# Performance work log

Hardware: AMD Instinct MI355X
Metric: run time of the kernel (lower is better)

Reference implementation:

```python
import jax, jax.numpy as jnp
import numpy as np

H = 4  # heads
L = 2  # num_layers


def _segment_softmax(alpha, seg, num_segments):
    # alpha: [E, H], seg: [E] destination node ids
    m = jax.ops.segment_max(alpha, seg, num_segments=num_segments)  # [N, H]
    m = jnp.where(jnp.isfinite(m), m, 0.0)
    ex = jnp.exp(alpha - m[seg])
    s = jax.ops.segment_sum(ex, seg, num_segments=num_segments)  # [N, H]
    return ex / (s[seg] + 1e-16)


def _conv(x, src, dst, edge_weight, edge_attr, wq, wk, wv, we, g, b):
    # x: [N, D]; edge_attr: [E, D]; one WePredConv layer (eval mode, no dropout)
    N, D = x.shape
    C = D // H
    q = (x @ wq).reshape(N, H, C)
    k = (x @ wk).reshape(N, H, C)
    v = (x @ wv).reshape(N, H, C)
    e = (edge_attr @ we).reshape(-1, H, C)
    alpha = (q[dst] + k[src] + e).sum(-1) / jnp.sqrt(jnp.float32(C))  # [E, H]
    alpha = alpha + g[None, :] * edge_weight[:, None]
    alpha = jax.nn.leaky_relu(alpha, negative_slope=0.2)
    alpha = _segment_softmax(alpha, dst, N)
    msg = v[src] * alpha[:, :, None]  # [E, H, C]
    out = jax.ops.segment_sum(msg, dst, num_segments=N).reshape(N, H * C)
    return out + b


def setup_inputs() -> dict:
    key = jax.random.key(0)
    ks = jax.random.split(key, 12)
    N, E, D, F, R = 50000, 400000, 128, 256, 200
    sc = 0.08  # ~xavier scale
    return {
        "entity": jnp.arange(N, dtype=jnp.int32),
        "edge_index": jax.random.randint(ks[0], (2, E), 0, N, dtype=jnp.int32),
        "edge_type": jax.random.randint(ks[1], (E,), 0, R, dtype=jnp.int32),
        "edge_weight": jax.random.uniform(ks[2], (E,), dtype=jnp.float32),
        "ent_table": jax.random.normal(ks[3], (N, F), dtype=jnp.float32),
        "proj_w": jax.random.normal(ks[4], (F, D), dtype=jnp.float32) * sc,
        "proj_b": jnp.zeros((D,), dtype=jnp.float32),
        "rel_emb": jax.random.normal(ks[5], (R, D), dtype=jnp.float32) * sc,
        "Wq": jax.random.normal(ks[6], (L, D, D), dtype=jnp.float32) * sc,
        "Wk": jax.random.normal(ks[7], (L, D, D), dtype=jnp.float32) * sc,
        "Wv": jax.random.normal(ks[8], (L, D, D), dtype=jnp.float32) * sc,
        "We": jax.random.normal(ks[9], (L, D, D), dtype=jnp.float32) * sc,
        "gate": jnp.ones((L, H), dtype=jnp.float32),
        "conv_bias": jnp.zeros((L, D), dtype=jnp.float32),
    }


def reference(entity, edge_index, edge_type, edge_weight, ent_table, proj_w,
              proj_b, rel_emb, Wq, Wk, Wv, We, gate, conv_bias):
    src, dst = edge_index[0], edge_index[1]
    x = ent_table[entity] @ proj_w + proj_b          # [N, D]
    edge_attr = rel_emb[edge_type]                   # [E, D]
    for l in range(L):
        x = _conv(x, src, dst, edge_weight, edge_attr,
                  Wq[l], Wk[l], Wv[l], We[l], gate[l], conv_bias[l])
        if l != L - 1:
            x = jax.nn.elu(x)
    return x
```

## Files before the change

### kernel.cpp

```cpp
#include <hip/hip_runtime.h>
#include <hip/hip_fp16.h>

#define HD 4
#define DD 128
#define CC 32
#define SCAN_B 64
#define SCAN_T 256

typedef float  f32x4   __attribute__((ext_vector_type(4)));
typedef short  short8v __attribute__((ext_vector_type(8)));

__device__ __forceinline__ unsigned short f2bf(float x) {
    unsigned u = __float_as_uint(x);
    return (unsigned short)((u + 0x7FFFu + ((u >> 16) & 1u)) >> 16);
}
__device__ __forceinline__ float bf2f(unsigned short h) {
    return __uint_as_float((unsigned)h << 16);
}

__global__ __launch_bounds__(256) void prep_kernel(
    const float* __restrict__ Wq, const float* __restrict__ Wk,
    const float* __restrict__ We, const float* __restrict__ rel,
    float* __restrict__ Wqh, float* __restrict__ Wkh,
    float* __restrict__ esum, int R)
{
    __shared__ float WehS[2][DD][HD];
    int tid = threadIdx.x;
    for (int i = tid; i < 2 * DD * HD; i += 256) {
        int l = i / (DD * HD);
        int d = (i / HD) % DD;
        int h = i % HD;
        const float* bq = Wq + ((size_t)l * DD + d) * DD + h * CC;
        const float* bk = Wk + ((size_t)l * DD + d) * DD + h * CC;
        const float* be = We + ((size_t)l * DD + d) * DD + h * CC;
        float sq = 0.f, sk = 0.f, se = 0.f;
        for (int c = 0; c < CC; ++c) { sq += bq[c]; sk += bk[c]; se += be[c]; }
        if (blockIdx.x == 0) { Wqh[i] = sq; Wkh[i] = sk; }
        WehS[l][d][h] = se;
    }
    __syncthreads();
    for (int i = blockIdx.x * 256 + tid; i < 2 * R * HD; i += gridDim.x * 256) {
        int l = i / (R * HD);
        int r = (i / HD) % R;
        int h = i % HD;
        const float* rp = rel + (size_t)r * DD;
        float a = 0.f;
        for (int d = 0; d < DD; ++d) a += rp[d] * WehS[l][d][h];
        esum[i] = a;
    }
}

__global__ __launch_bounds__(256) void prep_bt(
    const float* __restrict__ pw, const float* __restrict__ Wv,
    unsigned short* __restrict__ btp, unsigned short* __restrict__ btv)
{
    int t = blockIdx.x * 256 + threadIdx.x;
    if (t < 128 * 256) {
        int col = t >> 8, k = t & 255;
        btp[(size_t)col * 256 + k] = f2bf(pw[(size_t)k * DD + col]);
    } else if (t < 128 * 256 + 2 * DD * DD) {
        int u = t - 128 * 256;
        int l = u >> 14;
        int r = u & 16383;
        int col = r >> 7, k = r & 127;
        btv[((size_t)l * DD + col) * DD + k] = f2bf(Wv[((size_t)l * DD + k) * DD + col]);
    }
}

__global__ __launch_bounds__(256) void gemm_mfma(
    const float* __restrict__ A, const int* __restrict__ gather,
    const unsigned short* __restrict__ bth, const float* __restrict__ bias,
    const float* __restrict__ Wqh, const float* __restrict__ Wkh,
    float* __restrict__ Cf, __half* __restrict__ Chf,
    float* __restrict__ qs, float* __restrict__ ks,
    int M, int K)
{
    __shared__ unsigned short AhL[4][4][64][8];
    __shared__ unsigned short AlL[4][4][64][8];
    __shared__ unsigned short BhL[4][8][64][8];
    __shared__ float wq[DD * HD], wk[DD * HD];

    const int tid = threadIdx.x;
    const int wave = tid >> 6, lane = tid & 63;
    const int row0 = blockIdx.x * 64;

    if (qs) {
        for (int i = tid; i < DD * HD; i += 256) { wq[i] = Wqh[i]; wk[i] = Wkh[i]; }
    }

    const int sr = tid >> 2;
    const int sks = tid & 3;
    int arow = row0 + sr; if (arow >= M) arow = M - 1;
    const int ga = gather ? gather[arow] : arow;
    const float* Ap = A + (size_t)ga * K + sks * 32;

    const int bc = tid >> 1;
    const int bh2 = (tid & 1) * 64;
    const unsigned short* Bp = bth + (size_t)bc * K + bh2;
    const int bct = bc >> 4, bfr = bc & 15;

    const int fr = lane & 15, fg = lane >> 4;

    f32x4 acc[8] = {};
    float qp[4] = {}, kp[4] = {};

    const int nch = K >> 7;
    for (int ch = 0; ch < nch; ++ch) {
        float4 a[8];
#pragma unroll
        for (int i = 0; i < 8; ++i) a[i] = *(const float4*)(Ap + ch * 128 + i * 4);
        short8v b[8];
#pragma unroll
        for (int i = 0; i < 8; ++i) b[i] = *(const short8v*)(Bp + ch * 128 + i * 8);

        if (ch) __syncthreads();

        {
            const int rt = sr >> 4, frr = sr & 15;
#pragma unroll
            for (int g = 0; g < 4; ++g) {
                float vv[8] = {a[g*2].x, a[g*2].y, a[g*2].z, a[g*2].w,
                               a[g*2+1].x, a[g*2+1].y, a[g*2+1].z, a[g*2+1].w};
                short8v hv, lv;
#pragma unroll
                for (int j = 0; j < 8; ++j) {
                    unsigned short h = f2bf(vv[j]);
                    hv[j] = (short)h;
                    lv[j] = (short)f2bf(vv[j] - bf2f(h));
                }
                *(short8v*)&AhL[rt][sks][g * 16 + frr][0] = hv;
                *(short8v*)&AlL[rt][sks][g * 16 + frr][0] = lv;
            }
        }
        if (qs) {
#pragma unroll
            for (int i = 0; i < 8; ++i) {
                const float arr[4] = {a[i].x, a[i].y, a[i].z, a[i].w};
#pragma unroll
                for (int j = 0; j < 4; ++j) {
                    int d = ch * 128 + sks * 32 + i * 4 + j;
                    float4 qw = *(const float4*)&wq[d * HD];
                    float4 kw = *(const float4*)&wk[d * HD];
                    qp[0] += arr[j] * qw.x; qp[1] += arr[j] * qw.y;
                    qp[2] += arr[j] * qw.z; qp[3] += arr[j] * qw.w;
                    kp[0] += arr[j] * kw.x; kp[1] += arr[j] * kw.y;
                    kp[2] += arr[j] * kw.z; kp[3] += arr[j] * kw.w;
                }
            }
        }
#pragma unroll
        for (int g = 0; g < 8; ++g) {
            int kk = bh2 + g * 8;
            int ksb = kk >> 5, fgb = (kk & 31) >> 3;
            *(short8v*)&BhL[ksb][bct][fgb * 16 + bfr][0] = b[g];
        }
        __syncthreads();

#pragma unroll
        for (int ksc = 0; ksc < 4; ++ksc) {
            short8v ah = *(const short8v*)&AhL[wave][ksc][lane][0];
            short8v al = *(const short8v*)&AlL[wave][ksc][lane][0];
#pragma unroll
            for (int c = 0; c < 8; ++c) {
                short8v bh = *(const short8v*)&BhL[ksc][c][lane][0];
                acc[c] = __builtin_amdgcn_mfma_f32_16x16x32_bf16(ah, bh, acc[c], 0, 0, 0);
                acc[c] = __builtin_amdgcn_mfma_f32_16x16x32_bf16(al, bh, acc[c], 0, 0, 0);
            }
        }
    }

    if (qs) {
#pragma unroll
        for (int off = 1; off < 4; off <<= 1) {
#pragma unroll
            for (int h = 0; h < 4; ++h) {
                qp[h] += __shfl_xor(qp[h], off, 64);
                kp[h] += __shfl_xor(kp[h], off, 64);
            }
        }
        if ((tid & 3) == 0) {
            int row = row0 + sr;
            if (row < M) {
                *(float4*)&qs[(size_t)row * HD] = make_float4(qp[0], qp[1], qp[2], qp[3]);
                *(float4*)&ks[(size_t)row * HD] = make_float4(kp[0], kp[1], kp[2], kp[3]);
            }
        }
    }

#pragma unroll
    for (int c = 0; c < 8; ++c) {
        float bv = bias ? bias[c * 16 + fr] : 0.f;
#pragma unroll
        for (int i = 0; i < 4; ++i) {
            int row = row0 + wave * 16 + fg * 4 + i;
            if (row < M) {
                float val = acc[c][i] + bv;
                if (Chf) Chf[(size_t)row * DD + c * 16 + fr] = __float2half(val);
                else     Cf [(size_t)row * DD + c * 16 + fr] = val;
            }
        }
    }
}

__global__ __launch_bounds__(256) void csr_count(
    const int* __restrict__ dstv, int* __restrict__ deg, int E)
{
    int t = blockIdx.x * 256 + threadIdx.x;
    if (t < E) atomicAdd(&deg[dstv[t]], 1);
}

__global__ __launch_bounds__(SCAN_T) void scan_partial(
    const int* __restrict__ deg, int* __restrict__ blksum, int N)
{
    __shared__ int red[SCAN_T];
    int chunk = (N + SCAN_B - 1) / SCAN_B;
    int b0 = blockIdx.x * chunk;
    int e0 = b0 + chunk; if (e0 > N) e0 = N;
    int s = 0;
    for (int i = b0 + threadIdx.x; i < e0; i += SCAN_T) s += deg[i];
    red[threadIdx.x] = s;
    __syncthreads();
    for (int off = SCAN_T / 2; off > 0; off >>= 1) {
        if (threadIdx.x < off) red[threadIdx.x] += red[threadIdx.x + off];
        __syncthreads();
    }
    if (threadIdx.x == 0) blksum[blockIdx.x] = red[0];
}

__global__ __launch_bounds__(64) void scan_blk(
    const int* __restrict__ blksum, int* __restrict__ blkoff)
{
    if (threadIdx.x == 0) {
        int acc = 0;
        for (int i = 0; i < SCAN_B; ++i) { blkoff[i] = acc; acc += blksum[i]; }
        blkoff[SCAN_B] = acc;
    }
}

__global__ __launch_bounds__(SCAN_T) void scan_final(
    const int* __restrict__ deg, const int* __restrict__ blkoff,
    int* __restrict__ row_ptr, int N)
{
    __shared__ int tsum[SCAN_T];
    int tid = threadIdx.x;
    int chunk = (N + SCAN_B - 1) / SCAN_B;
    int b0 = blockIdx.x * chunk;
    int e0 = b0 + chunk; if (e0 > N) e0 = N;
    int tchunk = (chunk + SCAN_T - 1) / SCAN_T;
    int tb = b0 + tid * tchunk;
    int te = tb + tchunk; if (te > e0) te = e0;
    int s = 0;
    for (int i = tb; i < te; ++i) s += deg[i];
    tsum[tid] = s;
    __syncthreads();
    for (int off = 1; off < SCAN_T; off <<= 1) {
        int v = (tid >= off) ? tsum[tid - off] : 0;
        __syncthreads();
        tsum[tid] += v;
        __syncthreads();
    }
    int base = blkoff[blockIdx.x] + ((tid == 0) ? 0 : tsum[tid - 1]);
    for (int i = tb; i < te; ++i) { row_ptr[i] = base; base += deg[i]; }
    if (blockIdx.x == SCAN_B - 1 && tid == SCAN_T - 1) row_ptr[N] = blkoff[SCAN_B];
}

__global__ __launch_bounds__(256) void csr_scatter(
    const int* __restrict__ srcv, const int* __restrict__ dstv,
    const int* __restrict__ etype, const float* __restrict__ ew,
    const int* __restrict__ row_ptr, int* __restrict__ cursor,
    int4* __restrict__ c_pack, int E)
{
    int e = blockIdx.x * 256 + threadIdx.x;
    if (e >= E) return;
    int d = dstv[e];
    int p = row_ptr[d] + atomicAdd(&cursor[d], 1);
    c_pack[p] = make_int4(srcv[e], etype[e], __float_as_int(ew[e]), 0);
}

__global__ __launch_bounds__(256) void fused_conv(
    const int* __restrict__ row_ptr, const int4* __restrict__ c_pack,
    const float* __restrict__ qs, const float* __restrict__ ks,
    const float* __restrict__ esum, const float* __restrict__ gate,
    const __half* __restrict__ v, const float* __restrict__ bias,
    float* __restrict__ out, int N, int do_elu)
{
    int gw = (blockIdx.x * 256 + threadIdx.x) >> 6;
    int lane = threadIdx.x & 63;
    if (gw >= N) return;
    const int n = gw;
    const int beg = row_ptr[n], end = row_ptr[n + 1];
    const int c0 = lane * 2;
    const int h = lane >> 4;
    const float L2E = 1.4426950408889634f;
    const float scL = 0.17677669529663687f * 1.4426950408889634f;
    const float qh = qs[(size_t)n * HD + h];
    const float ghL = gate[h] * L2E;

    float num0 = 0.f, num1 = 0.f, den = 0.f;

    int j = beg;
    for (; j + 8 <= end; j += 8) {
        int4 p[8];
#pragma unroll
        for (int u = 0; u < 8; ++u) p[u] = c_pack[j + u];
        float kh[8], eh[8];
        float2 vv[8];
#pragma unroll
        for (int u = 0; u < 8; ++u) kh[u] = ks[(size_t)p[u].x * HD + h];
#pragma unroll
        for (int u = 0; u < 8; ++u) eh[u] = esum[(size_t)p[u].y * HD + h];
#pragma unroll
        for (int u = 0; u < 8; ++u)
            vv[u] = __half22float2(*(const __half2*)&v[(size_t)p[u].x * DD + c0]);
#pragma unroll
        for (int u = 0; u < 8; ++u) {
            float a = (qh + kh[u] + eh[u]) * scL + ghL * __int_as_float(p[u].z);
            a = a > 0.f ? a : 0.2f * a;
            float e = exp2f(a);
            den += e;
            num0 = fmaf(e, vv[u].x, num0);
            num1 = fmaf(e, vv[u].y, num1);
        }
    }
    for (; j + 4 <= end; j += 4) {
        int4 p0 = c_pack[j];
        int4 p1 = c_pack[j + 1];
        int4 p2 = c_pack[j + 2];
        int4 p3 = c_pack[j + 3];
        float kh0 = ks[(size_t)p0.x * HD + h];
        float kh1 = ks[(size_t)p1.x * HD + h];
        float kh2 = ks[(size_t)p2.x * HD + h];
        float kh3 = ks[(size_t)p3.x * HD + h];
        float eh0 = esum[(size_t)p0.y * HD + h];
        float eh1 = esum[(size_t)p1.y * HD + h];
        float eh2 = esum[(size_t)p2.y * HD + h];
        float eh3 = esum[(size_t)p3.y * HD + h];
        float2 vv0 = __half22float2(*(const __half2*)&v[(size_t)p0.x * DD + c0]);
        float2 vv1 = __half22float2(*(const __half2*)&v[(size_t)p1.x * DD + c0]);
        float2 vv2 = __half22float2(*(const __half2*)&v[(size_t)p2.x * DD + c0]);
        float2 vv3 = __half22float2(*(const __half2*)&v[(size_t)p3.x * DD + c0]);
        float a0 = (qh + kh0 + eh0) * scL + ghL * __int_as_float(p0.z);
        float a1 = (qh + kh1 + eh1) * scL + ghL * __int_as_float(p1.z);
        float a2 = (qh + kh2 + eh2) * scL + ghL * __int_as_float(p2.z);
        float a3 = (qh + kh3 + eh3) * scL + ghL * __int_as_float(p3.z);
        a0 = a0 > 0.f ? a0 : 0.2f * a0;
        a1 = a1 > 0.f ? a1 : 0.2f * a1;
        a2 = a2 > 0.f ? a2 : 0.2f * a2;
        a3 = a3 > 0.f ? a3 : 0.2f * a3;
        float e0 = exp2f(a0), e1 = exp2f(a1);
        float e2 = exp2f(a2), e3 = exp2f(a3);
        den += (e0 + e1) + (e2 + e3);
        num0 = fmaf(e0, vv0.x, num0); num1 = fmaf(e0, vv0.y, num1);
        num0 = fmaf(e1, vv1.x, num0); num1 = fmaf(e1, vv1.y, num1);
        num0 = fmaf(e2, vv2.x, num0); num1 = fmaf(e2, vv2.y, num1);
        num0 = fmaf(e3, vv3.x, num0); num1 = fmaf(e3, vv3.y, num1);
    }
    for (; j < end; ++j) {
        int4 cur = c_pack[j];
        float kh = ks[(size_t)cur.x * HD + h];
        float eh = esum[(size_t)cur.y * HD + h];
        float2 vv = __half22float2(*(const __half2*)&v[(size_t)cur.x * DD + c0]);
        float a = (qh + kh + eh) * scL + ghL * __int_as_float(cur.z);
        a = a > 0.f ? a : 0.2f * a;
        float e = exp2f(a);
        den += e;
        num0 = fmaf(e, vv.x, num0);
        num1 = fmaf(e, vv.y, num1);
    }

    float inv = 1.f / (den + 1e-16f);
    float r0 = num0 * inv + bias[c0];
    float r1 = num1 * inv + bias[c0 + 1];
    if (do_elu) {
        r0 = r0 > 0.f ? r0 : expm1f(r0);
        r1 = r1 > 0.f ? r1 : expm1f(r1);
    }
    *(float2*)&out[(size_t)n * DD + c0] = make_float2(r0, r1);
}

extern "C" void kernel_launch(void* const* d_in, const int* in_sizes, int n_in,
                              void* d_out, int out_size, void* d_ws, size_t ws_size,
                              hipStream_t stream)
{
    const int*   entity = (const int*)d_in[0];
    const int*   eidx   = (const int*)d_in[1];
    const int*   etype  = (const int*)d_in[2];
    const float* ew     = (const float*)d_in[3];
    const float* ent    = (const float*)d_in[4];
    const float* pw     = (const float*)d_in[5];
    const float* pb     = (const float*)d_in[6];
    const float* rel    = (const float*)d_in[7];
    const float* Wq     = (const float*)d_in[8];
    const float* Wk     = (const float*)d_in[9];
    const float* Wv     = (const float*)d_in[10];
    const float* We     = (const float*)d_in[11];
    const float* gate   = (const float*)d_in[12];
    const float* cb     = (const float*)d_in[13];

    const int N = in_sizes[0];
    const int E = in_sizes[2];
    const int F = in_sizes[4] / N;
    const int R = in_sizes[7] / DD;

    const int* srcv = eidx;
    const int* dstv = eidx + E;

    float* ws = (float*)d_ws;
    size_t o = 0;
    float* xbuf    = ws + o; o += (size_t)N * DD;
    __half* vbuf   = (__half*)(ws + o); o += (size_t)N * DD / 2;
    float* qs      = ws + o; o += (size_t)N * HD;
    float* ks      = ws + o; o += (size_t)N * HD;
    float* Wqh     = ws + o; o += 2 * DD * HD;
    float* Wkh     = ws + o; o += 2 * DD * HD;
    float* esum    = ws + o; o += (size_t)2 * R * HD;
    int*   deg     = (int*)(ws + o); o += N;
    int*   cursor  = (int*)(ws + o); o += N;
    int*   row_ptr = (int*)(ws + o); o += (size_t)N + 1;
    int*   blksum  = (int*)(ws + o); o += SCAN_B;
    int*   blkoff  = (int*)(ws + o); o += SCAN_B + 1;
    o = (o + 3) & ~(size_t)3;
    int4*  c_pack  = (int4*)(ws + o); o += (size_t)E * 4;
    unsigned short* btp = (unsigned short*)(ws + o); o += 128 * 256 / 2;
    unsigned short* btv = (unsigned short*)(ws + o); o += 2 * DD * DD / 2;

    prep_kernel<<<16, 256, 0, stream>>>(Wq, Wk, We, rel, Wqh, Wkh, esum, R);
    prep_bt<<<(128 * 256 + 2 * DD * DD + 255) / 256, 256, 0, stream>>>(
        pw, Wv, btp, btv);

    hipMemsetAsync(deg, 0, (size_t)2 * N * sizeof(int), stream);
    csr_count<<<(E + 255) / 256, 256, 0, stream>>>(dstv, deg, E);
    scan_partial<<<SCAN_B, SCAN_T, 0, stream>>>(deg, blksum, N);
    scan_blk<<<1, 64, 0, stream>>>(blksum, blkoff);
    scan_final<<<SCAN_B, SCAN_T, 0, stream>>>(deg, blkoff, row_ptr, N);
    csr_scatter<<<(E + 255) / 256, 256, 0, stream>>>(
        srcv, dstv, etype, ew, row_ptr, cursor, c_pack, E);

    const int gblk = (N + 63) / 64;
    gemm_mfma<<<gblk, 256, 0, stream>>>(
        ent, entity, btp, pb, nullptr, nullptr,
        xbuf, nullptr, nullptr, nullptr, N, F);

    const int fblk = (N + 3) / 4;
    for (int l = 0; l < 2; ++l) {
        gemm_mfma<<<gblk, 256, 0, stream>>>(
            xbuf, nullptr, btv + (size_t)l * DD * DD, nullptr,
            Wqh + l * DD * HD, Wkh + l * DD * HD,
            nullptr, vbuf, qs, ks, N, DD);
        fused_conv<<<fblk, 256, 0, stream>>>(
            row_ptr, c_pack, qs, ks, esum + (size_t)l * R * HD,
            gate + l * HD, vbuf, cb + l * DD,
            (l == 0) ? xbuf : (float*)d_out, N, (l == 0) ? 1 : 0);
    }
}
```

Measured before the change: 236.4 us.

## Precompute per-edge attention bias in a separate pass before fused conv

New measurement: 226.8 us. 4.1% less time.

```diff
diff --git a/kernel.cpp b/kernel.cpp
--- a/kernel.cpp
+++ b/kernel.cpp
@@ -268,19 +268,41 @@
     const int* __restrict__ srcv, const int* __restrict__ dstv,
     const int* __restrict__ etype, const float* __restrict__ ew,
     const int* __restrict__ row_ptr, int* __restrict__ cursor,
-    int4* __restrict__ c_pack, int E)
+    int4* __restrict__ c_pack, int* __restrict__ c_src, int E)
 {
     int e = blockIdx.x * 256 + threadIdx.x;
     if (e >= E) return;
     int d = dstv[e];
     int p = row_ptr[d] + atomicAdd(&cursor[d], 1);
     c_pack[p] = make_int4(srcv[e], etype[e], __float_as_int(ew[e]), 0);
+    c_src[p] = srcv[e];
+}
+
+__global__ __launch_bounds__(256) void edge_prep(
+    const int4* __restrict__ c_pack, const float* __restrict__ ks,
+    const float* __restrict__ esum, const float* __restrict__ gate,
+    float4* __restrict__ bedge, int E)
+{
+    int t = blockIdx.x * 256 + threadIdx.x;
+    if (t >= E) return;
+    const float L2E = 1.4426950408889634f;
+    const float scL = 0.17677669529663687f * 1.4426950408889634f;
+    int4 p = c_pack[t];
+    float w = __int_as_float(p.z);
+    float4 kv = *(const float4*)&ks[(size_t)p.x * HD];
+    float4 ev = *(const float4*)&esum[(size_t)p.y * HD];
+    float4 g  = *(const float4*)gate;
+    float4 b;
+    b.x = (kv.x + ev.x) * scL + g.x * L2E * w;
+    b.y = (kv.y + ev.y) * scL + g.y * L2E * w;
+    b.z = (kv.z + ev.z) * scL + g.z * L2E * w;
+    b.w = (kv.w + ev.w) * scL + g.w * L2E * w;
+    bedge[t] = b;
 }
 
 __global__ __launch_bounds__(256) void fused_conv(
-    const int* __restrict__ row_ptr, const int4* __restrict__ c_pack,
-    const float* __restrict__ qs, const float* __restrict__ ks,
-    const float* __restrict__ esum, const float* __restrict__ gate,
+    const int* __restrict__ row_ptr, const int* __restrict__ c_src,
+    const float* __restrict__ bedge, const float* __restrict__ qs,
     const __half* __restrict__ v, const float* __restrict__ bias,
     float* __restrict__ out, int N, int do_elu)
 {
@@ -291,30 +313,24 @@
     const int beg = row_ptr[n], end = row_ptr[n + 1];
     const int c0 = lane * 2;
     const int h = lane >> 4;
-    const float L2E = 1.4426950408889634f;
     const float scL = 0.17677669529663687f * 1.4426950408889634f;
-    const float qh = qs[(size_t)n * HD + h];
-    const float ghL = gate[h] * L2E;
+    const float qhs = qs[(size_t)n * HD + h] * scL;
 
     float num0 = 0.f, num1 = 0.f, den = 0.f;
 
     int j = beg;
     for (; j + 8 <= end; j += 8) {
-        int4 p[8];
-#pragma unroll
-        for (int u = 0; u < 8; ++u) p[u] = c_pack[j + u];
-        float kh[8], eh[8];
-        float2 vv[8];
-#pragma unroll
-        for (int u = 0; u < 8; ++u) kh[u] = ks[(size_t)p[u].x * HD + h];
-#pragma unroll
-        for (int u = 0; u < 8; ++u) eh[u] = esum[(size_t)p[u].y * HD + h];
+        int s[8]; float bh[8]; float2 vv[8];
+#pragma unroll
+        for (int u = 0; u < 8; ++u) s[u] = c_src[j + u];
+#pragma unroll
+        for (int u = 0; u < 8; ++u) bh[u] = bedge[(size_t)(j + u) * HD + h];
 #pragma unroll
         for (int u = 0; u < 8; ++u)
-            vv[u] = __half22float2(*(const __half2*)&v[(size_t)p[u].x * DD + c0]);
+            vv[u] = __half22float2(*(const __half2*)&v[(size_t)s[u] * DD + c0]);
 #pragma unroll
         for (int u = 0; u < 8; ++u) {
-            float a = (qh + kh[u] + eh[u]) * scL + ghL * __int_as_float(p[u].z);
+            float a = qhs + bh[u];
             a = a > 0.f ? a : 0.2f * a;
             float e = exp2f(a);
             den += e;
@@ -323,26 +339,16 @@
         }
     }
     for (; j + 4 <= end; j += 4) {
-        int4 p0 = c_pack[j];
-        int4 p1 = c_pack[j + 1];
-        int4 p2 = c_pack[j + 2];
-        int4 p3 = c_pack[j + 3];
-        float kh0 = ks[(size_t)p0.x * HD + h];
-        float kh1 = ks[(size_t)p1.x * HD + h];
-        float kh2 = ks[(size_t)p2.x * HD + h];
-        float kh3 = ks[(size_t)p3.x * HD + h];
-        float eh0 = esum[(size_t)p0.y * HD + h];
-        float eh1 = esum[(size_t)p1.y * HD + h];
-        float eh2 = esum[(size_t)p2.y * HD + h];
-        float eh3 = esum[(size_t)p3.y * HD + h];
-        float2 vv0 = __half22float2(*(const __half2*)&v[(size_t)p0.x * DD + c0]);
-        float2 vv1 = __half22float2(*(const __half2*)&v[(size_t)p1.x * DD + c0]);
-        float2 vv2 = __half22float2(*(const __half2*)&v[(size_t)p2.x * DD + c0]);
-        float2 vv3 = __half22float2(*(const __half2*)&v[(size_t)p3.x * DD + c0]);
-        float a0 = (qh + kh0 + eh0) * scL + ghL * __int_as_float(p0.z);
-        float a1 = (qh + kh1 + eh1) * scL + ghL * __int_as_float(p1.z);
-        float a2 = (qh + kh2 + eh2) * scL + ghL * __int_as_float(p2.z);
-        float a3 = (qh + kh3 + eh3) * scL + ghL * __int_as_float(p3.z);
+        int s0 = c_src[j], s1 = c_src[j + 1], s2 = c_src[j + 2], s3 = c_src[j + 3];
+        float b0 = bedge[(size_t)j * HD + h];
+        float b1 = bedge[(size_t)(j + 1) * HD + h];
+        float b2 = bedge[(size_t)(j + 2) * HD + h];
+        float b3 = bedge[(size_t)(j + 3) * HD + h];
+        float2 vv0 = __half22float2(*(const __half2*)&v[(size_t)s0 * DD + c0]);
+        float2 vv1 = __half22float2(*(const __half2*)&v[(size_t)s1 * DD + c0]);
+        float2 vv2 = __half22float2(*(const __half2*)&v[(size_t)s2 * DD + c0]);
+        float2 vv3 = __half22float2(*(const __half2*)&v[(size_t)s3 * DD + c0]);
+        float a0 = qhs + b0, a1 = qhs + b1, a2 = qhs + b2, a3 = qhs + b3;
         a0 = a0 > 0.f ? a0 : 0.2f * a0;
         a1 = a1 > 0.f ? a1 : 0.2f * a1;
         a2 = a2 > 0.f ? a2 : 0.2f * a2;
@@ -356,11 +362,10 @@
         num0 = fmaf(e3, vv3.x, num0); num1 = fmaf(e3, vv3.y, num1);
     }
     for (; j < end; ++j) {
-        int4 cur = c_pack[j];
-        float kh = ks[(size_t)cur.x * HD + h];
-        float eh = esum[(size_t)cur.y * HD + h];
-        float2 vv = __half22float2(*(const __half2*)&v[(size_t)cur.x * DD + c0]);
-        float a = (qh + kh + eh) * scL + ghL * __int_as_float(cur.z);
+        int s = c_src[j];
+        float b = bedge[(size_t)j * HD + h];
+        float2 vv = __half22float2(*(const __half2*)&v[(size_t)s * DD + c0]);
+        float a = qhs + b;
         a = a > 0.f ? a : 0.2f * a;
         float e = exp2f(a);
         den += e;
@@ -421,6 +426,9 @@
     int*   blkoff  = (int*)(ws + o); o += SCAN_B + 1;
     o = (o + 3) & ~(size_t)3;
     int4*  c_pack  = (int4*)(ws + o); o += (size_t)E * 4;
+    int*   c_src   = (int*)(ws + o); o += E;
+    o = (o + 3) & ~(size_t)3;
+    float4* bedge  = (float4*)(ws + o); o += (size_t)E * 4;
     unsigned short* btp = (unsigned short*)(ws + o); o += 128 * 256 / 2;
     unsigned short* btv = (unsigned short*)(ws + o); o += 2 * DD * DD / 2;
 
@@ -434,7 +442,7 @@
     scan_blk<<<1, 64, 0, stream>>>(blksum, blkoff);
     scan_final<<<SCAN_B, SCAN_T, 0, stream>>>(deg, blkoff, row_ptr, N);
     csr_scatter<<<(E + 255) / 256, 256, 0, stream>>>(
-        srcv, dstv, etype, ew, row_ptr, cursor, c_pack, E);
+        srcv, dstv, etype, ew, row_ptr, cursor, c_pack, c_src, E);
 
     const int gblk = (N + 63) / 64;
     gemm_mfma<<<gblk, 256, 0, stream>>>(
@@ -442,14 +450,16 @@
         xbuf, nullptr, nullptr, nullptr, N, F);
 
     const int fblk = (N + 3) / 4;
+    const int eblk = (E + 255) / 256;
     for (int l = 0; l < 2; ++l) {
         gemm_mfma<<<gblk, 256, 0, stream>>>(
             xbuf, nullptr, btv + (size_t)l * DD * DD, nullptr,
             Wqh + l * DD * HD, Wkh + l * DD * HD,
             nullptr, vbuf, qs, ks, N, DD);
+        edge_prep<<<eblk, 256, 0, stream>>>(
+            c_pack, ks, esum + (size_t)l * R * HD, gate + l * HD, bedge, E);
         fused_conv<<<fblk, 256, 0, stream>>>(
-            row_ptr, c_pack, qs, ks, esum + (size_t)l * R * HD,
-            gate + l * HD, vbuf, cb + l * DD,
+            row_ptr, c_src, (const float*)bedge, qs, vbuf, cb + l * DD,
             (l == 0) ? xbuf : (float*)d_out, N, (l == 0) ? 1 : 0);
     }
 }
```
